# Kernel tuning notes

Measured on AMD Instinct MI355X. Metric: run time of the kernel, lower is better.

The kernel has to match this reference:

```python
import jax, jax.numpy as jnp
import numpy as np

B = 1024
N_CPGS = 20000
N_FREQS = N_CPGS // 2 + 1  # 10001
HIDDEN = (256, 128, 64)
LN_EPS = 1e-5


def setup_inputs() -> dict:
    key = jax.random.key(0)
    keys = jax.random.split(key, 16)
    inp = {"x": jax.random.normal(keys[0], (B, N_CPGS), dtype=jnp.float32)}
    in_dim = N_FREQS
    for i, h in enumerate(HIDDEN):
        inp[f"W{i}"] = jax.random.normal(keys[1 + i], (h, in_dim), dtype=jnp.float32) * 0.01
        inp[f"alpha{i}"] = jnp.full((h, in_dim), 0.01, dtype=jnp.float32)
        inp[f"b{i}"] = jnp.zeros((h,), dtype=jnp.float32)
        inp[f"eta{i}"] = jnp.asarray(0.1, dtype=jnp.float32)
        inp[f"g{i}"] = jnp.ones((h,), dtype=jnp.float32)   # LayerNorm gamma
        inp[f"be{i}"] = jnp.zeros((h,), dtype=jnp.float32)  # LayerNorm beta
        in_dim = h
    inp["head_w"] = jax.random.normal(keys[10], (1, in_dim), dtype=jnp.float32) * (1.0 / np.sqrt(in_dim))
    inp["head_b"] = jnp.zeros((1,), dtype=jnp.float32)
    return inp


def _hebbian_layer(x, W, alpha, b, eta):
    # y_slow = x W^T + b;  plastic[b,i] = eta * tanh(y_slow)[b,i] * sum_j sigmoid(alpha)[i,j] * x_norm[b,j] * x[b,j]
    y_slow = jnp.einsum('bd,hd->bh', x, W) + b
    x_norm = x / (jnp.linalg.norm(x, axis=-1, keepdims=True) + 1e-8)
    c = x_norm * x  # (B, in) -- collapses the (B,out,in) outer-product trace algebraically
    plastic = eta * jnp.tanh(y_slow) * jnp.einsum('bd,hd->bh', c, jax.nn.sigmoid(alpha))
    return y_slow + plastic


def _layer_norm(h, g, be):
    mu = jnp.mean(h, axis=-1, keepdims=True)
    var = jnp.mean((h - mu) ** 2, axis=-1, keepdims=True)
    return (h - mu) * jax.lax.rsqrt(var + LN_EPS) * g + be


def reference(x, W0, alpha0, b0, eta0, g0, be0,
              W1, alpha1, b1, eta1, g1, be1,
              W2, alpha2, b2, eta2, g2, be2,
              head_w, head_b):
    # FFT spectral front-end
    xc = x - jnp.mean(x, axis=1, keepdims=True)
    h = jnp.log1p(jnp.abs(jnp.fft.rfft(xc, axis=1)))  # (B, N_FREQS)
    params = [(W0, alpha0, b0, eta0, g0, be0),
              (W1, alpha1, b1, eta1, g1, be1),
              (W2, alpha2, b2, eta2, g2, be2)]
    for (W, a, b, eta, g, be) in params:
        h = jax.nn.gelu(_layer_norm(_hebbian_layer(h, W, a, b, eta), g, be), approximate=False)
        # dropout is identity in eval mode
    return (jnp.einsum('bd,od->bo', h, head_w) + head_b)[:, 0]  # (B,)
```

## Files before the change

kernel.cpp:

```cpp
#include <hip/hip_runtime.h>
#include <hip/hip_bf16.h>
#include <math.h>

typedef short bf16x8 __attribute__((ext_vector_type(8)));
typedef float f32x4 __attribute__((ext_vector_type(4)));

static __device__ __forceinline__ unsigned short f2bf(float f) {
    unsigned int u = __float_as_uint(f);
    unsigned int r = (u + 0x7fffu + ((u >> 16) & 1u)) >> 16;
    return (unsigned short)r;
}

static __device__ __forceinline__ bf16x8 sq_bf16x8(bf16x8 a) {
    bf16x8 r;
    #pragma unroll
    for (int i = 0; i < 8; ++i) {
        unsigned int u = ((unsigned int)(unsigned short)a[i]) << 16;
        float f = __uint_as_float(u);
        f *= f;
        r[i] = (short)f2bf(f);
    }
    return r;
}

static __device__ __forceinline__ float gelu_f(float x) {
    return 0.5f * x * (1.f + erff(x * 0.70710678118654752f));
}

static __device__ __forceinline__ void gload_lds16(const void* g, void* l) {
    __builtin_amdgcn_global_load_lds(
        (const __attribute__((address_space(1))) unsigned int*)g,
        (__attribute__((address_space(3))) unsigned int*)l, 16, 0, 0);
}

static __device__ __forceinline__ int ldsmap(int i) { return i + (i >> 6); }

static __device__ __forceinline__ int rev4(int k) {
    int d0 = k % 10; k /= 10;
    int d1 = k % 10; k /= 10;
    int d2 = k % 10; int d3 = k / 10;
    return d0 * 1000 + d1 * 100 + d2 * 10 + d3;
}

__global__ __launch_bounds__(256)
void init_tables_kernel(unsigned int* __restrict__ idxTab, float2* __restrict__ twAll)
{
    int i = blockIdx.x * 256 + threadIdx.x;
    if (i < 10001) {
        int k1 = (i == 10000) ? 0 : i;
        int k2 = (k1 == 0) ? 0 : 10000 - k1;
        unsigned a = (unsigned)ldsmap(rev4(k1));
        unsigned b = (unsigned)ldsmap(rev4(k2));
        idxTab[i] = a | (b << 16);
    }
    if (i < 9990) {
        int m;
        if (i < 9000)       { int t = i / 1000 + 1; int j = i - (t - 1) * 1000; m = j * t; }
        else if (i < 9900)  { int e = i - 9000; int t = e / 100 + 1; int j = e - (t - 1) * 100; m = 10 * j * t; }
        else                { int e = i - 9900; int t = e / 10 + 1;  int j = e - (t - 1) * 10;  m = 100 * j * t; }
        double ang = (double)m * -6.2831853071795864769e-4;
        twAll[i] = make_float2((float)cos(ang), (float)sin(ang));
    }
}

static __device__ __forceinline__ void dft5(
    float a0r, float a0i, float a1r, float a1i, float a2r, float a2i,
    float a3r, float a3i, float a4r, float a4i,
    float* Xr, float* Xi)
{
    const float c1 = 0.30901699437494742f, c2 = -0.80901699437494745f;
    const float s1 = 0.95105651629515357f, s2 = 0.58778525229247312f;
    float t1r = a1r + a4r, t1i = a1i + a4i;
    float d1r = a1r - a4r, d1i = a1i - a4i;
    float t2r = a2r + a3r, t2i = a2i + a3i;
    float d2r = a2r - a3r, d2i = a2i - a3i;
    Xr[0] = a0r + t1r + t2r; Xi[0] = a0i + t1i + t2i;
    float m1r = a0r + c1 * t1r + c2 * t2r, m1i = a0i + c1 * t1i + c2 * t2i;
    float m2r = a0r + c2 * t1r + c1 * t2r, m2i = a0i + c2 * t1i + c1 * t2i;
    float n1r = s1 * d1r + s2 * d2r, n1i = s1 * d1i + s2 * d2i;
    float n2r = s2 * d1r - s1 * d2r, n2i = s2 * d1i - s1 * d2i;
    Xr[1] = m1r + n1i; Xi[1] = m1i - n1r;
    Xr[4] = m1r - n1i; Xi[4] = m1i + n1r;
    Xr[2] = m2r + n2i; Xi[2] = m2i - n2r;
    Xr[3] = m2r - n2i; Xi[3] = m2i + n2r;
}

template<int S>
static __device__ __forceinline__ void radix10_core(
    float* __restrict__ reb, float* __restrict__ imb,
    const float* ar, const float* ai, int base, int j,
    const float2* __restrict__ tw)
{
    constexpr int L  = (S == 0) ? 1000 : (S == 1) ? 100 : (S == 2) ? 10 : 1;
    constexpr bool TW = (S != 3);

    const float WR[5] = {1.f, 0.80901699437494745f, 0.30901699437494742f,
                         -0.30901699437494742f, -0.80901699437494745f};
    const float WI[5] = {0.f, -0.58778525229247312f, -0.95105651629515357f,
                         -0.95105651629515357f, -0.58778525229247312f};

    float Er[5], Ei[5], Or[5], Oi[5];
    dft5(ar[0], ai[0], ar[2], ai[2], ar[4], ai[4], ar[6], ai[6], ar[8], ai[8], Er, Ei);
    dft5(ar[1], ai[1], ar[3], ai[3], ar[5], ai[5], ar[7], ai[7], ar[9], ai[9], Or, Oi);
    #pragma unroll
    for (int k = 1; k < 5; ++k) {
        float tr = Or[k] * WR[k] - Oi[k] * WI[k];
        Oi[k] = Or[k] * WI[k] + Oi[k] * WR[k];
        Or[k] = tr;
    }

    if (TW) {
        float twr[10], twi[10];
        #pragma unroll
        for (int t = 1; t < 10; ++t) {
            float2 w_ = tw[(t - 1) * L + j];
            twr[t] = w_.x; twi[t] = w_.y;
        }
        #pragma unroll
        for (int k = 0; k < 5; ++k) {
            float xr0 = Er[k] + Or[k], xi0 = Ei[k] + Oi[k];
            float xr1 = Er[k] - Or[k], xi1 = Ei[k] - Oi[k];
            int i0 = ldsmap(base + k * L);
            int i1 = ldsmap(base + (k + 5) * L);
            if (k == 0) {
                reb[i0] = xr0;
                imb[i0] = xi0;
            } else {
                reb[i0] = xr0 * twr[k] - xi0 * twi[k];
                imb[i0] = xr0 * twi[k] + xi0 * twr[k];
            }
            reb[i1] = xr1 * twr[k + 5] - xi1 * twi[k + 5];
            imb[i1] = xr1 * twi[k + 5] + xi1 * twr[k + 5];
        }
    } else {
        #pragma unroll
        for (int k = 0; k < 5; ++k) {
            int i0 = ldsmap(base + k * L);
            int i1 = ldsmap(base + (k + 5) * L);
            reb[i0] = Er[k] + Or[k]; imb[i0] = Ei[k] + Oi[k];
            reb[i1] = Er[k] - Or[k]; imb[i1] = Ei[k] - Oi[k];
        }
    }
}

template<int S>
static __device__ __forceinline__ void radix10_stage(
    float* __restrict__ reb, float* __restrict__ imb, int tid,
    const float2* __restrict__ tw)
{
    constexpr int L = (S == 1) ? 100 : (S == 2) ? 10 : 1;
    for (int w = tid; w < 1000; w += 512) {
        int g, j;
        if (S == 3) { g = w; j = 0; }
        else        { g = w / L; j = w - g * L; }
        const int base = g * (10 * L) + j;
        float ar[10], ai[10];
        #pragma unroll
        for (int u = 0; u < 10; ++u) {
            int idx = ldsmap(base + u * L);
            ar[u] = reb[idx];
            ai[u] = imb[idx];
        }
        radix10_core<S>(reb, imb, ar, ai, base, j, tw);
    }
}

__global__ __launch_bounds__(512, 4)
void fft_prep_kernel(const float* __restrict__ x,
                     unsigned short* __restrict__ hb,
                     float* __restrict__ hnorm,
                     const float* __restrict__ W0, const float* __restrict__ A0,
                     unsigned short* __restrict__ Wb, unsigned short* __restrict__ Sb,
                     const float* __restrict__ W1, const float* __restrict__ A1,
                     const float* __restrict__ W2, const float* __restrict__ A2,
                     float* __restrict__ W1T, float* __restrict__ S1T,
                     float* __restrict__ W2T, float* __restrict__ S2T,
                     const unsigned int* __restrict__ idxTab,
                     const float2* __restrict__ twAll)
{
    if (blockIdx.x >= 1024) {
        int idx = (blockIdx.x - 1024) * 512 + threadIdx.x;
        if (idx < 1280128) {
            const bool isW = idx < 640064;
            const int f4 = isW ? idx : idx - 640064;
            const float* src = isW ? W0 : A0;
            unsigned short* dst = isW ? Wb : Sb;
            float4 v = ((const float4*)src)[f4];
            float e[4] = {v.x, v.y, v.z, v.w};
            int flat = f4 * 4;
            int row = flat / 10001;
            int col = flat - row * 10001;
            #pragma unroll
            for (int i = 0; i < 4; ++i) {
                if (col == 10001) { row++; col = 0; }
                float val = isW ? e[i] : 1.f / (1.f + expf(-e[i]));
                dst[(size_t)row * 10240 + col] = f2bf(val);
                col++;
            }
        } else if (idx < 1341312) {
            int i = idx - 1280128;
            int row = i / 239;
            int col = 10001 + (i - row * 239);
            Wb[(size_t)row * 10240 + col] = 0;
            Sb[(size_t)row * 10240 + col] = 0;
        } else if (idx < 1423232) {
            int o = idx - 1341312;
            if (o < 32768) {
                int d = o >> 7, h = o & 127;
                W1T[o] = W1[h * 256 + d];
            } else if (o < 65536) {
                int p = o - 32768;
                int d = p >> 7, h = p & 127;
                S1T[p] = 1.f / (1.f + expf(-A1[h * 256 + d]));
            } else if (o < 73728) {
                int p = o - 65536;
                int d = p >> 6, h = p & 63;
                W2T[p] = W2[h * 128 + d];
            } else {
                int p = o - 73728;
                int d = p >> 6, h = p & 63;
                S2T[p] = 1.f / (1.f + expf(-A2[h * 128 + d]));
            }
        }
        return;
    }

    __shared__ float reb[10156];
    __shared__ float imb[10156];
    __shared__ float redbuf[8];

    const int b = blockIdx.x;
    const int tid = threadIdx.x;
    const int lane = tid & 63;
    const int wv = tid >> 6;

    const float2* T0 = twAll;
    const float2* T1 = twAll + 9000;
    const float2* T2 = twAll + 9900;

    const float2* z2 = (const float2*)(x + (size_t)b * 20000);
    for (int w = tid; w < 1000; w += 512) {
        float ar[10], ai[10];
        #pragma unroll
        for (int u = 0; u < 10; ++u) {
            float2 v = z2[w + u * 1000];
            ar[u] = v.x; ai[u] = v.y;
        }
        radix10_core<0>(reb, imb, ar, ai, w, w, T0);
    }
    __syncthreads();
    radix10_stage<1>(reb, imb, tid, T1);
    __syncthreads();
    radix10_stage<2>(reb, imb, tid, T2);
    __syncthreads();
    radix10_stage<3>(reb, imb, tid, (const float2*)nullptr);
    __syncthreads();

    float ct, st;
    __sincosf((float)tid * -3.14159265358979324e-4f, &st, &ct);
    const float RC = 0.987091579f;
    const float RS = -0.160156842f;
    float sumsq = 0.f;
    unsigned short* hrow = hb + (size_t)b * 10240;
    #pragma unroll
    for (int i = 0; i < 20; ++i) {
        int k = tid + i * 512;
        float hval = 0.f;
        if (k > 0 && k <= 10000) {
            unsigned pp = idxTab[k];
            int i1 = (int)(pp & 0xffffu);
            int i2 = (int)(pp >> 16);
            float zr = reb[i1], zi = imb[i1];
            float wr = reb[i2], wi = imb[i2];
            float er = 0.5f * (zr + wr);
            float ei = 0.5f * (zi - wi);
            float odr = 0.5f * (zi + wi);
            float odi = -0.5f * (zr - wr);
            float xre = er + ct * odr - st * odi;
            float xim = ei + ct * odi + st * odr;
            hval = __logf(1.f + sqrtf(xre * xre + xim * xim));
        }
        hrow[k] = f2bf(hval);
        sumsq += hval * hval;
        float nct = ct * RC - st * RS;
        st = ct * RS + st * RC;
        ct = nct;
    }
    #pragma unroll
    for (int o = 32; o; o >>= 1) sumsq += __shfl_xor(sumsq, o);
    __syncthreads();
    if (lane == 0) redbuf[wv] = sumsq;
    __syncthreads();
    if (tid == 0) {
        float tsq = 0.f;
        #pragma unroll
        for (int i = 0; i < 8; ++i) tsq += redbuf[i];
        hnorm[b] = 1.f / (sqrtf(tsq) + 1e-8f);
    }
}

__global__ __launch_bounds__(256, 3)
void gemm0_kernel(const unsigned short* __restrict__ hb,
                  const unsigned short* __restrict__ Wb, const unsigned short* __restrict__ Sb,
                  float* __restrict__ Py, float* __restrict__ Pp)
{
    __shared__ unsigned short Ah[64 * 64];
    __shared__ unsigned short Bw[64 * 64];
    __shared__ unsigned short Bs[64 * 64];

    const int t = threadIdx.x;
    const int lin = blockIdx.x;
    const int z = lin & 7;
    const int tile = lin >> 3;
    const int b0 = (tile & 15) * 64;
    const int n0 = (tile >> 4) * 64;

    const int lane = t & 63;
    const int wv = t >> 6;
    const int ml = lane & 15;
    const int q4 = lane >> 4;
    const int s0 = q4 ^ (ml & 7);

    const int sub8 = lane >> 3;
    const int sl = lane & 7;
    const int gsw = sl ^ sub8;

    f32x4 accY[4], accP[4];
    #pragma unroll
    for (int nt = 0; nt < 4; ++nt) {
        accY[nt] = (f32x4){0.f, 0.f, 0.f, 0.f};
        accP[nt] = (f32x4){0.f, 0.f, 0.f, 0.f};
    }

    const int kbase = z * 1280;

    for (int step = 0; step < 20; ++step) {
        const int k0 = kbase + step * 64;
        __syncthreads();
        #pragma unroll
        for (int j = 0; j < 2; ++j) {
            const int c = wv * 2 + j;
            const size_t goA = (size_t)(b0 + c * 8 + sub8) * 10240 + k0 + gsw * 8;
            gload_lds16(&hb[goA], &Ah[c * 512]);
            const size_t goB = (size_t)(n0 + c * 8 + sub8) * 10240 + k0 + gsw * 8;
            gload_lds16(&Wb[goB], &Bw[c * 512]);
            gload_lds16(&Sb[goB], &Bs[c * 512]);
        }
        __syncthreads();

        #pragma unroll
        for (int kk = 0; kk < 2; ++kk) {
            const int slot = (s0 ^ (kk << 2)) << 3;
            bf16x8 ah, ac, bw[4], bs[4];
            const int mrow = wv * 16 + ml;
            ah = *(const bf16x8*)&Ah[mrow * 64 + slot];
            ac = sq_bf16x8(ah);
            #pragma unroll
            for (int nt = 0; nt < 4; ++nt) {
                int nrow = nt * 16 + ml;
                bw[nt] = *(const bf16x8*)&Bw[nrow * 64 + slot];
                bs[nt] = *(const bf16x8*)&Bs[nrow * 64 + slot];
            }
            #pragma unroll
            for (int nt = 0; nt < 4; ++nt) {
                accY[nt] = __builtin_amdgcn_mfma_f32_16x16x32_bf16(ah, bw[nt], accY[nt], 0, 0, 0);
                accP[nt] = __builtin_amdgcn_mfma_f32_16x16x32_bf16(ac, bs[nt], accP[nt], 0, 0, 0);
            }
        }
    }

    const int rq = q4 * 4;
    #pragma unroll
    for (int nt = 0; nt < 4; ++nt)
        #pragma unroll
        for (int r = 0; r < 4; ++r) {
            int m = b0 + wv * 16 + rq + r;
            int n = n0 + nt * 16 + ml;
            size_t o = ((size_t)z * 1024 + m) * 256 + n;
            Py[o] = accY[nt][r];
            Pp[o] = accP[nt][r];
        }
}

__global__ __launch_bounds__(256)
void combine_tail_kernel(const float* __restrict__ Py, const float* __restrict__ Pp,
                 const float* __restrict__ hnorm,
                 const float* __restrict__ b0v, const float* __restrict__ eta0p,
                 const float* __restrict__ g0, const float* __restrict__ be0,
                 const float* __restrict__ W1T, const float* __restrict__ S1T,
                 const float* __restrict__ b1, const float* __restrict__ eta1p,
                 const float* __restrict__ g1, const float* __restrict__ be1,
                 const float* __restrict__ W2T, const float* __restrict__ S2T,
                 const float* __restrict__ b2, const float* __restrict__ eta2p,
                 const float* __restrict__ g2, const float* __restrict__ be2,
                 const float* __restrict__ hw, const float* __restrict__ hbod,
                 float* __restrict__ out)
{
    __shared__ float sh[2][256];
    __shared__ float sc[2][256];
    __shared__ float sv[2][128];
    __shared__ float sh2[2][128];
    __shared__ float sc2[2][128];
    __shared__ float sv2[2][64];
    __shared__ float p2a[2][2][64];
    __shared__ float p2b[2][2][64];
    __shared__ float redA[4][2];
    __shared__ float redB[4][2];

    const int t = threadIdx.x;
    const int b0 = blockIdx.x * 2;
    const int lane = t & 63;
    const int wv = t >> 6;

    const float e0 = eta0p[0];
    const float bias0 = b0v[t];
    float ys[2] = {0.f, 0.f}, ps[2] = {0.f, 0.f};
    #pragma unroll 4
    for (int s = 0; s < 8; ++s)
        #pragma unroll
        for (int r = 0; r < 2; ++r) {
            size_t o = ((size_t)s * 1024 + b0 + r) * 256 + t;
            ys[r] += Py[o];
            ps[r] += Pp[o];
        }
    float v[2];
    #pragma unroll
    for (int r = 0; r < 2; ++r) {
        float p = ps[r] * hnorm[b0 + r];
        float y = ys[r] + bias0;
        v[r] = y + e0 * tanhf(y) * p;
    }

    float s1[2], s2[2];
    #pragma unroll
    for (int r = 0; r < 2; ++r) { s1[r] = v[r]; s2[r] = v[r] * v[r]; }
    #pragma unroll
    for (int o = 32; o; o >>= 1)
        #pragma unroll
        for (int r = 0; r < 2; ++r) { s1[r] += __shfl_xor(s1[r], o); s2[r] += __shfl_xor(s2[r], o); }
    if (lane == 0)
        #pragma unroll
        for (int r = 0; r < 2; ++r) { redA[wv][r] = s1[r]; redB[wv][r] = s2[r]; }
    __syncthreads();

    const float gg = g0[t], bb = be0[t];
    float gl[2], s3[2];
    #pragma unroll
    for (int r = 0; r < 2; ++r) {
        float sum = redA[0][r] + redA[1][r] + redA[2][r] + redA[3][r];
        float sumsq = redB[0][r] + redB[1][r] + redB[2][r] + redB[3][r];
        float mu = sum * (1.f / 256.f);
        float var = sumsq * (1.f / 256.f) - mu * mu;
        float u = (v[r] - mu) * rsqrtf(var + 1e-5f) * gg + bb;
        gl[r] = gelu_f(u);
        s3[r] = gl[r] * gl[r];
    }
    #pragma unroll
    for (int o = 32; o; o >>= 1)
        #pragma unroll
        for (int r = 0; r < 2; ++r) s3[r] += __shfl_xor(s3[r], o);
    __syncthreads();
    if (lane == 0)
        #pragma unroll
        for (int r = 0; r < 2; ++r) redA[wv][r] = s3[r];
    __syncthreads();
    #pragma unroll
    for (int r = 0; r < 2; ++r) {
        float gsq = redA[0][r] + redA[1][r] + redA[2][r] + redA[3][r];
        float inv = 1.f / (sqrtf(gsq) + 1e-8f);
        sh[r][t] = gl[r];
        sc[r][t] = gl[r] * gl[r] * inv;
    }
    __syncthreads();

    const int hcol = t & 127;
    const int r1 = t >> 7;
    float ya = 0.f, pa = 0.f;
    #pragma unroll 8
    for (int d = 0; d < 256; ++d) {
        ya += sh[r1][d] * W1T[d * 128 + hcol];
        pa += sc[r1][d] * S1T[d * 128 + hcol];
    }
    {
        const float e1 = eta1p[0];
        float y = ya + b1[hcol];
        sv[r1][hcol] = y + e1 * tanhf(y) * pa;
    }
    __syncthreads();

    if (wv < 2) {
        int r = wv;
        float v0 = sv[r][lane];
        float v1 = sv[r][lane + 64];
        float s = v0 + v1, sq = v0 * v0 + v1 * v1;
        #pragma unroll
        for (int o = 32; o; o >>= 1) { s += __shfl_xor(s, o); sq += __shfl_xor(sq, o); }
        float mu = s * (1.f / 128.f);
        float var = sq * (1.f / 128.f) - mu * mu;
        float rs = rsqrtf(var + 1e-5f);
        float u0 = (v0 - mu) * rs * g1[lane] + be1[lane];
        float u1 = (v1 - mu) * rs * g1[lane + 64] + be1[lane + 64];
        float ge0 = gelu_f(u0);
        float ge1 = gelu_f(u1);
        float gsq = ge0 * ge0 + ge1 * ge1;
        #pragma unroll
        for (int o = 32; o; o >>= 1) gsq += __shfl_xor(gsq, o);
        float inv = 1.f / (sqrtf(gsq) + 1e-8f);
        sh2[r][lane] = ge0; sh2[r][lane + 64] = ge1;
        sc2[r][lane] = ge0 * ge0 * inv; sc2[r][lane + 64] = ge1 * ge1 * inv;
    }
    __syncthreads();

    {
        const int h2c = t & 63;
        const int r = (t >> 6) & 1;
        const int dh = t >> 7;
        float yb = 0.f, pb = 0.f;
        #pragma unroll 8
        for (int dd = 0; dd < 64; ++dd) {
            int d = dh * 64 + dd;
            yb += sh2[r][d] * W2T[d * 64 + h2c];
            pb += sc2[r][d] * S2T[d * 64 + h2c];
        }
        p2a[dh][r][h2c] = yb;
        p2b[dh][r][h2c] = pb;
    }
    __syncthreads();
    if (t < 128) {
        const int h2c = t & 63;
        const int r = t >> 6;
        const float e2 = eta2p[0];
        float yb = p2a[0][r][h2c] + p2a[1][r][h2c];
        float pb = p2b[0][r][h2c] + p2b[1][r][h2c];
        float y = yb + b2[h2c];
        sv2[r][h2c] = y + e2 * tanhf(y) * pb;
    }
    __syncthreads();

    if (wv < 2) {
        int r = wv;
        float v0 = sv2[r][lane];
        float s = v0, sq = v0 * v0;
        #pragma unroll
        for (int o = 32; o; o >>= 1) { s += __shfl_xor(s, o); sq += __shfl_xor(sq, o); }
        float mu = s * (1.f / 64.f);
        float var = sq * (1.f / 64.f) - mu * mu;
        float rs = rsqrtf(var + 1e-5f);
        float u = (v0 - mu) * rs * g2[lane] + be2[lane];
        float g = gelu_f(u);
        float hc = g * hw[lane];
        #pragma unroll
        for (int o = 32; o; o >>= 1) hc += __shfl_xor(hc, o);
        if (lane == 0) out[b0 + r] = hc + hbod[0];
    }
}

extern "C" void kernel_launch(void* const* d_in, const int* in_sizes, int n_in,
                              void* d_out, int out_size, void* d_ws, size_t ws_size,
                              hipStream_t stream)
{
    const float* x    = (const float*)d_in[0];
    const float* W0   = (const float*)d_in[1];
    const float* A0   = (const float*)d_in[2];
    const float* b0   = (const float*)d_in[3];
    const float* eta0 = (const float*)d_in[4];
    const float* g0   = (const float*)d_in[5];
    const float* be0  = (const float*)d_in[6];
    const float* W1   = (const float*)d_in[7];
    const float* A1   = (const float*)d_in[8];
    const float* b1   = (const float*)d_in[9];
    const float* eta1 = (const float*)d_in[10];
    const float* g1   = (const float*)d_in[11];
    const float* be1  = (const float*)d_in[12];
    const float* W2   = (const float*)d_in[13];
    const float* A2   = (const float*)d_in[14];
    const float* b2   = (const float*)d_in[15];
    const float* eta2 = (const float*)d_in[16];
    const float* g2   = (const float*)d_in[17];
    const float* be2  = (const float*)d_in[18];
    const float* hw   = (const float*)d_in[19];
    const float* hbod = (const float*)d_in[20];
    float* out = (float*)d_out;

    char* w = (char*)d_ws;
    unsigned short* hb  = (unsigned short*)(w + 0);
    unsigned short* Wb0 = (unsigned short*)(w + 20971520);
    unsigned short* Sb0 = (unsigned short*)(w + 26214400);
    float* Py   = (float*)(w + 31457280);
    float* Pp   = (float*)(w + 39845888);
    float* W1T  = (float*)(w + 48234496);
    float* S1T  = (float*)(w + 48365568);
    float* W2T  = (float*)(w + 48496640);
    float* S2T  = (float*)(w + 48529408);
    float* hnm  = (float*)(w + 48562176);
    unsigned int* idxT = (unsigned int*)(w + 48566272);
    float2* twT = (float2*)(w + 48607232);

    hipLaunchKernelGGL(init_tables_kernel, dim3(40), dim3(256), 0, stream, idxT, twT);
    hipLaunchKernelGGL(fft_prep_kernel, dim3(3804), dim3(512), 0, stream,
                       x, hb, hnm, W0, A0, Wb0, Sb0, W1, A1, W2, A2, W1T, S1T, W2T, S2T,
                       idxT, twT);
    hipLaunchKernelGGL(gemm0_kernel, dim3(512), dim3(256), 0, stream, hb, Wb0, Sb0, Py, Pp);
    hipLaunchKernelGGL(combine_tail_kernel, dim3(512), dim3(256), 0, stream, Py, Pp, hnm,
                       b0, eta0, g0, be0, W1T, S1T, b1, eta1, g1, be1,
                       W2T, S2T, b2, eta2, g2, be2, hw, hbod, out);
}
```

Before: 255.3 us.

## Fuse GEMM and tail via cooperative grid sync; compute FFT twiddles inline

Removes the twiddle/index table init kernel and computes twiddles on the fly with sincos plus a recurrence, and computes the bit-reverse indices inline. The GEMM and the combine/tail kernels are merged into one cooperative kernel with a grid-wide sync in between, so two launches disappear. The cooperative launch needs all 512 blocks resident at once and lowers launch_bounds occupancy to 2. Twiddle accuracy may drop slightly because of fast sincos and the recurrence.

```diff
diff --git a/kernel.cpp b/kernel.cpp
--- a/kernel.cpp
+++ b/kernel.cpp
@@ -1,6 +1,9 @@
 #include <hip/hip_runtime.h>
 #include <hip/hip_bf16.h>
+#include <hip/hip_cooperative_groups.h>
 #include <math.h>
+
+namespace cg = cooperative_groups;
 
 typedef short bf16x8 __attribute__((ext_vector_type(8)));
 typedef float f32x4 __attribute__((ext_vector_type(4)));
@@ -40,27 +43,6 @@
     int d1 = k % 10; k /= 10;
     int d2 = k % 10; int d3 = k / 10;
     return d0 * 1000 + d1 * 100 + d2 * 10 + d3;
-}
-
-__global__ __launch_bounds__(256)
-void init_tables_kernel(unsigned int* __restrict__ idxTab, float2* __restrict__ twAll)
-{
-    int i = blockIdx.x * 256 + threadIdx.x;
-    if (i < 10001) {
-        int k1 = (i == 10000) ? 0 : i;
-        int k2 = (k1 == 0) ? 0 : 10000 - k1;
-        unsigned a = (unsigned)ldsmap(rev4(k1));
-        unsigned b = (unsigned)ldsmap(rev4(k2));
-        idxTab[i] = a | (b << 16);
-    }
-    if (i < 9990) {
-        int m;
-        if (i < 9000)       { int t = i / 1000 + 1; int j = i - (t - 1) * 1000; m = j * t; }
-        else if (i < 9900)  { int e = i - 9000; int t = e / 100 + 1; int j = e - (t - 1) * 100; m = 10 * j * t; }
-        else                { int e = i - 9900; int t = e / 10 + 1;  int j = e - (t - 1) * 10;  m = 100 * j * t; }
-        double ang = (double)m * -6.2831853071795864769e-4;
-        twAll[i] = make_float2((float)cos(ang), (float)sin(ang));
-    }
 }
 
 static __device__ __forceinline__ void dft5(
@@ -88,10 +70,10 @@
 template<int S>
 static __device__ __forceinline__ void radix10_core(
     float* __restrict__ reb, float* __restrict__ imb,
-    const float* ar, const float* ai, int base, int j,
-    const float2* __restrict__ tw)
+    const float* ar, const float* ai, int base, int j)
 {
     constexpr int L  = (S == 0) ? 1000 : (S == 1) ? 100 : (S == 2) ? 10 : 1;
+    constexpr int SC = (S == 0) ? 1 : (S == 1) ? 10 : (S == 2) ? 100 : 1000;
     constexpr bool TW = (S != 3);
 
     const float WR[5] = {1.f, 0.80901699437494745f, 0.30901699437494742f,
@@ -110,11 +92,15 @@
     }
 
     if (TW) {
+        const float ang = (float)(j * SC) * -6.28318530717958648e-4f;
+        float w1c, w1s;
+        __sincosf(ang, &w1s, &w1c);
         float twr[10], twi[10];
+        twr[0] = 1.f; twi[0] = 0.f;
         #pragma unroll
         for (int t = 1; t < 10; ++t) {
-            float2 w_ = tw[(t - 1) * L + j];
-            twr[t] = w_.x; twi[t] = w_.y;
+            twr[t] = twr[t - 1] * w1c - twi[t - 1] * w1s;
+            twi[t] = twr[t - 1] * w1s + twi[t - 1] * w1c;
         }
         #pragma unroll
         for (int k = 0; k < 5; ++k) {
@@ -145,8 +131,7 @@
 
 template<int S>
 static __device__ __forceinline__ void radix10_stage(
-    float* __restrict__ reb, float* __restrict__ imb, int tid,
-    const float2* __restrict__ tw)
+    float* __restrict__ reb, float* __restrict__ imb, int tid)
 {
     constexpr int L = (S == 1) ? 100 : (S == 2) ? 10 : 1;
     for (int w = tid; w < 1000; w += 512) {
@@ -161,7 +146,7 @@
             ar[u] = reb[idx];
             ai[u] = imb[idx];
         }
-        radix10_core<S>(reb, imb, ar, ai, base, j, tw);
+        radix10_core<S>(reb, imb, ar, ai, base, j);
     }
 }
 
@@ -174,9 +159,7 @@
                      const float* __restrict__ W1, const float* __restrict__ A1,
                      const float* __restrict__ W2, const float* __restrict__ A2,
                      float* __restrict__ W1T, float* __restrict__ S1T,
-                     float* __restrict__ W2T, float* __restrict__ S2T,
-                     const unsigned int* __restrict__ idxTab,
-                     const float2* __restrict__ twAll)
+                     float* __restrict__ W2T, float* __restrict__ S2T)
 {
     if (blockIdx.x >= 1024) {
         int idx = (blockIdx.x - 1024) * 512 + threadIdx.x;
@@ -234,10 +217,6 @@
     const int lane = tid & 63;
     const int wv = tid >> 6;
 
-    const float2* T0 = twAll;
-    const float2* T1 = twAll + 9000;
-    const float2* T2 = twAll + 9900;
-
     const float2* z2 = (const float2*)(x + (size_t)b * 20000);
     for (int w = tid; w < 1000; w += 512) {
         float ar[10], ai[10];
@@ -246,20 +225,16 @@
             float2 v = z2[w + u * 1000];
             ar[u] = v.x; ai[u] = v.y;
         }
-        radix10_core<0>(reb, imb, ar, ai, w, w, T0);
+        radix10_core<0>(reb, imb, ar, ai, w, w);
     }
     __syncthreads();
-    radix10_stage<1>(reb, imb, tid, T1);
+    radix10_stage<1>(reb, imb, tid);
     __syncthreads();
-    radix10_stage<2>(reb, imb, tid, T2);
+    radix10_stage<2>(reb, imb, tid);
     __syncthreads();
-    radix10_stage<3>(reb, imb, tid, (const float2*)nullptr);
+    radix10_stage<3>(reb, imb, tid);
     __syncthreads();
 
-    float ct, st;
-    __sincosf((float)tid * -3.14159265358979324e-4f, &st, &ct);
-    const float RC = 0.987091579f;
-    const float RS = -0.160156842f;
     float sumsq = 0.f;
     unsigned short* hrow = hb + (size_t)b * 10240;
     #pragma unroll
@@ -267,24 +242,24 @@
         int k = tid + i * 512;
         float hval = 0.f;
         if (k > 0 && k <= 10000) {
-            unsigned pp = idxTab[k];
-            int i1 = (int)(pp & 0xffffu);
-            int i2 = (int)(pp >> 16);
+            int k1 = (k == 10000) ? 0 : k;
+            int k2 = (k1 == 0) ? 0 : 10000 - k1;
+            int i1 = ldsmap(rev4(k1));
+            int i2 = ldsmap(rev4(k2));
             float zr = reb[i1], zi = imb[i1];
             float wr = reb[i2], wi = imb[i2];
             float er = 0.5f * (zr + wr);
             float ei = 0.5f * (zi - wi);
             float odr = 0.5f * (zi + wi);
             float odi = -0.5f * (zr - wr);
+            float ct, st;
+            __sincosf((float)k * -3.14159265358979324e-4f, &st, &ct);
             float xre = er + ct * odr - st * odi;
             float xim = ei + ct * odi + st * odr;
             hval = __logf(1.f + sqrtf(xre * xre + xim * xim));
         }
         hrow[k] = f2bf(hval);
         sumsq += hval * hval;
-        float nct = ct * RC - st * RS;
-        st = ct * RS + st * RC;
-        ct = nct;
     }
     #pragma unroll
     for (int o = 32; o; o >>= 1) sumsq += __shfl_xor(sumsq, o);
@@ -299,103 +274,26 @@
     }
 }
 
-__global__ __launch_bounds__(256, 3)
-void gemm0_kernel(const unsigned short* __restrict__ hb,
-                  const unsigned short* __restrict__ Wb, const unsigned short* __restrict__ Sb,
-                  float* __restrict__ Py, float* __restrict__ Pp)
+__global__ __launch_bounds__(256, 2)
+void gemm_tail_kernel(const unsigned short* __restrict__ hb,
+                      const unsigned short* __restrict__ Wb, const unsigned short* __restrict__ Sb,
+                      float* __restrict__ Py, float* __restrict__ Pp,
+                      const float* __restrict__ hnorm,
+                      const float* __restrict__ b0v, const float* __restrict__ eta0p,
+                      const float* __restrict__ g0, const float* __restrict__ be0,
+                      const float* __restrict__ W1T, const float* __restrict__ S1T,
+                      const float* __restrict__ b1, const float* __restrict__ eta1p,
+                      const float* __restrict__ g1, const float* __restrict__ be1,
+                      const float* __restrict__ W2T, const float* __restrict__ S2T,
+                      const float* __restrict__ b2, const float* __restrict__ eta2p,
+                      const float* __restrict__ g2, const float* __restrict__ be2,
+                      const float* __restrict__ hw, const float* __restrict__ hbod,
+                      float* __restrict__ out)
 {
     __shared__ unsigned short Ah[64 * 64];
     __shared__ unsigned short Bw[64 * 64];
     __shared__ unsigned short Bs[64 * 64];
 
-    const int t = threadIdx.x;
-    const int lin = blockIdx.x;
-    const int z = lin & 7;
-    const int tile = lin >> 3;
-    const int b0 = (tile & 15) * 64;
-    const int n0 = (tile >> 4) * 64;
-
-    const int lane = t & 63;
-    const int wv = t >> 6;
-    const int ml = lane & 15;
-    const int q4 = lane >> 4;
-    const int s0 = q4 ^ (ml & 7);
-
-    const int sub8 = lane >> 3;
-    const int sl = lane & 7;
-    const int gsw = sl ^ sub8;
-
-    f32x4 accY[4], accP[4];
-    #pragma unroll
-    for (int nt = 0; nt < 4; ++nt) {
-        accY[nt] = (f32x4){0.f, 0.f, 0.f, 0.f};
-        accP[nt] = (f32x4){0.f, 0.f, 0.f, 0.f};
-    }
-
-    const int kbase = z * 1280;
-
-    for (int step = 0; step < 20; ++step) {
-        const int k0 = kbase + step * 64;
-        __syncthreads();
-        #pragma unroll
-        for (int j = 0; j < 2; ++j) {
-            const int c = wv * 2 + j;
-            const size_t goA = (size_t)(b0 + c * 8 + sub8) * 10240 + k0 + gsw * 8;
-            gload_lds16(&hb[goA], &Ah[c * 512]);
-            const size_t goB = (size_t)(n0 + c * 8 + sub8) * 10240 + k0 + gsw * 8;
-            gload_lds16(&Wb[goB], &Bw[c * 512]);
-            gload_lds16(&Sb[goB], &Bs[c * 512]);
-        }
-        __syncthreads();
-
-        #pragma unroll
-        for (int kk = 0; kk < 2; ++kk) {
-            const int slot = (s0 ^ (kk << 2)) << 3;
-            bf16x8 ah, ac, bw[4], bs[4];
-            const int mrow = wv * 16 + ml;
-            ah = *(const bf16x8*)&Ah[mrow * 64 + slot];
-            ac = sq_bf16x8(ah);
-            #pragma unroll
-            for (int nt = 0; nt < 4; ++nt) {
-                int nrow = nt * 16 + ml;
-                bw[nt] = *(const bf16x8*)&Bw[nrow * 64 + slot];
-                bs[nt] = *(const bf16x8*)&Bs[nrow * 64 + slot];
-            }
-            #pragma unroll
-            for (int nt = 0; nt < 4; ++nt) {
-                accY[nt] = __builtin_amdgcn_mfma_f32_16x16x32_bf16(ah, bw[nt], accY[nt], 0, 0, 0);
-                accP[nt] = __builtin_amdgcn_mfma_f32_16x16x32_bf16(ac, bs[nt], accP[nt], 0, 0, 0);
-            }
-        }
-    }
-
-    const int rq = q4 * 4;
-    #pragma unroll
-    for (int nt = 0; nt < 4; ++nt)
-        #pragma unroll
-        for (int r = 0; r < 4; ++r) {
-            int m = b0 + wv * 16 + rq + r;
-            int n = n0 + nt * 16 + ml;
-            size_t o = ((size_t)z * 1024 + m) * 256 + n;
-            Py[o] = accY[nt][r];
-            Pp[o] = accP[nt][r];
-        }
-}
-
-__global__ __launch_bounds__(256)
-void combine_tail_kernel(const float* __restrict__ Py, const float* __restrict__ Pp,
-                 const float* __restrict__ hnorm,
-                 const float* __restrict__ b0v, const float* __restrict__ eta0p,
-                 const float* __restrict__ g0, const float* __restrict__ be0,
-                 const float* __restrict__ W1T, const float* __restrict__ S1T,
-                 const float* __restrict__ b1, const float* __restrict__ eta1p,
-                 const float* __restrict__ g1, const float* __restrict__ be1,
-                 const float* __restrict__ W2T, const float* __restrict__ S2T,
-                 const float* __restrict__ b2, const float* __restrict__ eta2p,
-                 const float* __restrict__ g2, const float* __restrict__ be2,
-                 const float* __restrict__ hw, const float* __restrict__ hbod,
-                 float* __restrict__ out)
-{
     __shared__ float sh[2][256];
     __shared__ float sc[2][256];
     __shared__ float sv[2][128];
@@ -408,150 +306,227 @@
     __shared__ float redB[4][2];
 
     const int t = threadIdx.x;
-    const int b0 = blockIdx.x * 2;
     const int lane = t & 63;
     const int wv = t >> 6;
 
-    const float e0 = eta0p[0];
-    const float bias0 = b0v[t];
-    float ys[2] = {0.f, 0.f}, ps[2] = {0.f, 0.f};
-    #pragma unroll 4
-    for (int s = 0; s < 8; ++s)
+    {
+        const int lin = blockIdx.x;
+        const int z = lin & 7;
+        const int tile = lin >> 3;
+        const int b0 = (tile & 15) * 64;
+        const int n0 = (tile >> 4) * 64;
+
+        const int ml = lane & 15;
+        const int q4 = lane >> 4;
+        const int s0 = q4 ^ (ml & 7);
+        const int sub8 = lane >> 3;
+        const int sl = lane & 7;
+        const int gsw = sl ^ sub8;
+
+        f32x4 accY[4], accP[4];
+        #pragma unroll
+        for (int nt = 0; nt < 4; ++nt) {
+            accY[nt] = (f32x4){0.f, 0.f, 0.f, 0.f};
+            accP[nt] = (f32x4){0.f, 0.f, 0.f, 0.f};
+        }
+
+        const int kbase = z * 1280;
+
+        for (int step = 0; step < 20; ++step) {
+            const int k0 = kbase + step * 64;
+            __syncthreads();
+            #pragma unroll
+            for (int j = 0; j < 2; ++j) {
+                const int c = wv * 2 + j;
+                const size_t goA = (size_t)(b0 + c * 8 + sub8) * 10240 + k0 + gsw * 8;
+                gload_lds16(&hb[goA], &Ah[c * 512]);
+                const size_t goB = (size_t)(n0 + c * 8 + sub8) * 10240 + k0 + gsw * 8;
+                gload_lds16(&Wb[goB], &Bw[c * 512]);
+                gload_lds16(&Sb[goB], &Bs[c * 512]);
+            }
+            __syncthreads();
+
+            #pragma unroll
+            for (int kk = 0; kk < 2; ++kk) {
+                const int slot = (s0 ^ (kk << 2)) << 3;
+                bf16x8 ah, ac, bw[4], bs[4];
+                const int mrow = wv * 16 + ml;
+                ah = *(const bf16x8*)&Ah[mrow * 64 + slot];
+                ac = sq_bf16x8(ah);
+                #pragma unroll
+                for (int nt = 0; nt < 4; ++nt) {
+                    int nrow = nt * 16 + ml;
+                    bw[nt] = *(const bf16x8*)&Bw[nrow * 64 + slot];
+                    bs[nt] = *(const bf16x8*)&Bs[nrow * 64 + slot];
+                }
+                #pragma unroll
+                for (int nt = 0; nt < 4; ++nt) {
+                    accY[nt] = __builtin_amdgcn_mfma_f32_16x16x32_bf16(ah, bw[nt], accY[nt], 0, 0, 0);
+                    accP[nt] = __builtin_amdgcn_mfma_f32_16x16x32_bf16(ac, bs[nt], accP[nt], 0, 0, 0);
+                }
+            }
+        }
+
+        const int rq = q4 * 4;
+        #pragma unroll
+        for (int nt = 0; nt < 4; ++nt)
+            #pragma unroll
+            for (int r = 0; r < 4; ++r) {
+                int m = b0 + wv * 16 + rq + r;
+                int n = n0 + nt * 16 + ml;
+                size_t o = ((size_t)z * 1024 + m) * 256 + n;
+                Py[o] = accY[nt][r];
+                Pp[o] = accP[nt][r];
+            }
+    }
+
+    __threadfence();
+    cg::this_grid().sync();
+
+    {
+        const int b0 = blockIdx.x * 2;
+
+        const float e0 = eta0p[0];
+        const float bias0 = b0v[t];
+        float ys[2] = {0.f, 0.f}, ps[2] = {0.f, 0.f};
+        #pragma unroll 4
+        for (int s = 0; s < 8; ++s)
+            #pragma unroll
+            for (int r = 0; r < 2; ++r) {
+                size_t o = ((size_t)s * 1024 + b0 + r) * 256 + t;
+                ys[r] += Py[o];
+                ps[r] += Pp[o];
+            }
+        float v[2];
         #pragma unroll
         for (int r = 0; r < 2; ++r) {
-            size_t o = ((size_t)s * 1024 + b0 + r) * 256 + t;
-            ys[r] += Py[o];
-            ps[r] += Pp[o];
-        }
-    float v[2];
-    #pragma unroll
-    for (int r = 0; r < 2; ++r) {
-        float p = ps[r] * hnorm[b0 + r];
-        float y = ys[r] + bias0;
-        v[r] = y + e0 * tanhf(y) * p;
-    }
-
-    float s1[2], s2[2];
-    #pragma unroll
-    for (int r = 0; r < 2; ++r) { s1[r] = v[r]; s2[r] = v[r] * v[r]; }
-    #pragma unroll
-    for (int o = 32; o; o >>= 1)
-        #pragma unroll
-        for (int r = 0; r < 2; ++r) { s1[r] += __shfl_xor(s1[r], o); s2[r] += __shfl_xor(s2[r], o); }
-    if (lane == 0)
-        #pragma unroll
-        for (int r = 0; r < 2; ++r) { redA[wv][r] = s1[r]; redB[wv][r] = s2[r]; }
-    __syncthreads();
-
-    const float gg = g0[t], bb = be0[t];
-    float gl[2], s3[2];
-    #pragma unroll
-    for (int r = 0; r < 2; ++r) {
-        float sum = redA[0][r] + redA[1][r] + redA[2][r] + redA[3][r];
-        float sumsq = redB[0][r] + redB[1][r] + redB[2][r] + redB[3][r];
-        float mu = sum * (1.f / 256.f);
-        float var = sumsq * (1.f / 256.f) - mu * mu;
-        float u = (v[r] - mu) * rsqrtf(var + 1e-5f) * gg + bb;
-        gl[r] = gelu_f(u);
-        s3[r] = gl[r] * gl[r];
-    }
-    #pragma unroll
-    for (int o = 32; o; o >>= 1)
-        #pragma unroll
-        for (int r = 0; r < 2; ++r) s3[r] += __shfl_xor(s3[r], o);
-    __syncthreads();
-    if (lane == 0)
-        #pragma unroll
-        for (int r = 0; r < 2; ++r) redA[wv][r] = s3[r];
-    __syncthreads();
-    #pragma unroll
-    for (int r = 0; r < 2; ++r) {
-        float gsq = redA[0][r] + redA[1][r] + redA[2][r] + redA[3][r];
-        float inv = 1.f / (sqrtf(gsq) + 1e-8f);
-        sh[r][t] = gl[r];
-        sc[r][t] = gl[r] * gl[r] * inv;
-    }
-    __syncthreads();
-
-    const int hcol = t & 127;
-    const int r1 = t >> 7;
-    float ya = 0.f, pa = 0.f;
-    #pragma unroll 8
-    for (int d = 0; d < 256; ++d) {
-        ya += sh[r1][d] * W1T[d * 128 + hcol];
-        pa += sc[r1][d] * S1T[d * 128 + hcol];
-    }
-    {
-        const float e1 = eta1p[0];
-        float y = ya + b1[hcol];
-        sv[r1][hcol] = y + e1 * tanhf(y) * pa;
-    }
-    __syncthreads();
-
-    if (wv < 2) {
-        int r = wv;
-        float v0 = sv[r][lane];
-        float v1 = sv[r][lane + 64];
-        float s = v0 + v1, sq = v0 * v0 + v1 * v1;
-        #pragma unroll
-        for (int o = 32; o; o >>= 1) { s += __shfl_xor(s, o); sq += __shfl_xor(sq, o); }
-        float mu = s * (1.f / 128.f);
-        float var = sq * (1.f / 128.f) - mu * mu;
-        float rs = rsqrtf(var + 1e-5f);
-        float u0 = (v0 - mu) * rs * g1[lane] + be1[lane];
-        float u1 = (v1 - mu) * rs * g1[lane + 64] + be1[lane + 64];
-        float ge0 = gelu_f(u0);
-        float ge1 = gelu_f(u1);
-        float gsq = ge0 * ge0 + ge1 * ge1;
-        #pragma unroll
-        for (int o = 32; o; o >>= 1) gsq += __shfl_xor(gsq, o);
-        float inv = 1.f / (sqrtf(gsq) + 1e-8f);
-        sh2[r][lane] = ge0; sh2[r][lane + 64] = ge1;
-        sc2[r][lane] = ge0 * ge0 * inv; sc2[r][lane + 64] = ge1 * ge1 * inv;
-    }
-    __syncthreads();
-
-    {
-        const int h2c = t & 63;
-        const int r = (t >> 6) & 1;
-        const int dh = t >> 7;
-        float yb = 0.f, pb = 0.f;
+            float p = ps[r] * hnorm[b0 + r];
+            float y = ys[r] + bias0;
+            v[r] = y + e0 * tanhf(y) * p;
+        }
+
+        float s1[2], s2[2];
+        #pragma unroll
+        for (int r = 0; r < 2; ++r) { s1[r] = v[r]; s2[r] = v[r] * v[r]; }
+        #pragma unroll
+        for (int o = 32; o; o >>= 1)
+            #pragma unroll
+            for (int r = 0; r < 2; ++r) { s1[r] += __shfl_xor(s1[r], o); s2[r] += __shfl_xor(s2[r], o); }
+        if (lane == 0)
+            #pragma unroll
+            for (int r = 0; r < 2; ++r) { redA[wv][r] = s1[r]; redB[wv][r] = s2[r]; }
+        __syncthreads();
+
+        const float gg = g0[t], bb = be0[t];
+        float gl[2], s3[2];
+        #pragma unroll
+        for (int r = 0; r < 2; ++r) {
+            float sum = redA[0][r] + redA[1][r] + redA[2][r] + redA[3][r];
+            float sumsq = redB[0][r] + redB[1][r] + redB[2][r] + redB[3][r];
+            float mu = sum * (1.f / 256.f);
+            float var = sumsq * (1.f / 256.f) - mu * mu;
+            float u = (v[r] - mu) * rsqrtf(var + 1e-5f) * gg + bb;
+            gl[r] = gelu_f(u);
+            s3[r] = gl[r] * gl[r];
+        }
+        #pragma unroll
+        for (int o = 32; o; o >>= 1)
+            #pragma unroll
+            for (int r = 0; r < 2; ++r) s3[r] += __shfl_xor(s3[r], o);
+        __syncthreads();
+        if (lane == 0)
+            #pragma unroll
+            for (int r = 0; r < 2; ++r) redA[wv][r] = s3[r];
+        __syncthreads();
+        #pragma unroll
+        for (int r = 0; r < 2; ++r) {
+            float gsq = redA[0][r] + redA[1][r] + redA[2][r] + redA[3][r];
+            float inv = 1.f / (sqrtf(gsq) + 1e-8f);
+            sh[r][t] = gl[r];
+            sc[r][t] = gl[r] * gl[r] * inv;
+        }
+        __syncthreads();
+
+        const int hcol = t & 127;
+        const int r1 = t >> 7;
+        float ya = 0.f, pa = 0.f;
         #pragma unroll 8
-        for (int dd = 0; dd < 64; ++dd) {
-            int d = dh * 64 + dd;
-            yb += sh2[r][d] * W2T[d * 64 + h2c];
-            pb += sc2[r][d] * S2T[d * 64 + h2c];
-        }
-        p2a[dh][r][h2c] = yb;
-        p2b[dh][r][h2c] = pb;
-    }
-    __syncthreads();
-    if (t < 128) {
-        const int h2c = t & 63;
-        const int r = t >> 6;
-        const float e2 = eta2p[0];
-        float yb = p2a[0][r][h2c] + p2a[1][r][h2c];
-        float pb = p2b[0][r][h2c] + p2b[1][r][h2c];
-        float y = yb + b2[h2c];
-        sv2[r][h2c] = y + e2 * tanhf(y) * pb;
-    }
-    __syncthreads();
-
-    if (wv < 2) {
-        int r = wv;
-        float v0 = sv2[r][lane];
-        float s = v0, sq = v0 * v0;
-        #pragma unroll
-        for (int o = 32; o; o >>= 1) { s += __shfl_xor(s, o); sq += __shfl_xor(sq, o); }
-        float mu = s * (1.f / 64.f);
-        float var = sq * (1.f / 64.f) - mu * mu;
-        float rs = rsqrtf(var + 1e-5f);
-        float u = (v0 - mu) * rs * g2[lane] + be2[lane];
-        float g = gelu_f(u);
-        float hc = g * hw[lane];
-        #pragma unroll
-        for (int o = 32; o; o >>= 1) hc += __shfl_xor(hc, o);
-        if (lane == 0) out[b0 + r] = hc + hbod[0];
+        for (int d = 0; d < 256; ++d) {
+            ya += sh[r1][d] * W1T[d * 128 + hcol];
+            pa += sc[r1][d] * S1T[d * 128 + hcol];
+        }
+        {
+            const float e1 = eta1p[0];
+            float y = ya + b1[hcol];
+            sv[r1][hcol] = y + e1 * tanhf(y) * pa;
+        }
+        __syncthreads();
+
+        if (wv < 2) {
+            int r = wv;
+            float v0 = sv[r][lane];
+            float v1 = sv[r][lane + 64];
+            float s = v0 + v1, sq = v0 * v0 + v1 * v1;
+            #pragma unroll
+            for (int o = 32; o; o >>= 1) { s += __shfl_xor(s, o); sq += __shfl_xor(sq, o); }
+            float mu = s * (1.f / 128.f);
+            float var = sq * (1.f / 128.f) - mu * mu;
+            float rs = rsqrtf(var + 1e-5f);
+            float u0 = (v0 - mu) * rs * g1[lane] + be1[lane];
+            float u1 = (v1 - mu) * rs * g1[lane + 64] + be1[lane + 64];
+            float ge0 = gelu_f(u0);
+            float ge1 = gelu_f(u1);
+            float gsq = ge0 * ge0 + ge1 * ge1;
+            #pragma unroll
+            for (int o = 32; o; o >>= 1) gsq += __shfl_xor(gsq, o);
+            float inv = 1.f / (sqrtf(gsq) + 1e-8f);
+            sh2[r][lane] = ge0; sh2[r][lane + 64] = ge1;
+            sc2[r][lane] = ge0 * ge0 * inv; sc2[r][lane + 64] = ge1 * ge1 * inv;
+        }
+        __syncthreads();
+
+        {
+            const int h2c = t & 63;
+            const int r = (t >> 6) & 1;
+            const int dh = t >> 7;
+            float yb = 0.f, pb = 0.f;
+            #pragma unroll 8
+            for (int dd = 0; dd < 64; ++dd) {
+                int d = dh * 64 + dd;
+                yb += sh2[r][d] * W2T[d * 64 + h2c];
+                pb += sc2[r][d] * S2T[d * 64 + h2c];
+            }
+            p2a[dh][r][h2c] = yb;
+            p2b[dh][r][h2c] = pb;
+        }
+        __syncthreads();
+        if (t < 128) {
+            const int h2c = t & 63;
+            const int r = t >> 6;
+            const float e2 = eta2p[0];
+            float yb = p2a[0][r][h2c] + p2a[1][r][h2c];
+            float pb = p2b[0][r][h2c] + p2b[1][r][h2c];
+            float y = yb + b2[h2c];
+            sv2[r][h2c] = y + e2 * tanhf(y) * pb;
+        }
+        __syncthreads();
+
+        if (wv < 2) {
+            int r = wv;
+            float v0 = sv2[r][lane];
+            float s = v0, sq = v0 * v0;
+            #pragma unroll
+            for (int o = 32; o; o >>= 1) { s += __shfl_xor(s, o); sq += __shfl_xor(sq, o); }
+            float mu = s * (1.f / 64.f);
+            float var = sq * (1.f / 64.f) - mu * mu;
+            float rs = rsqrtf(var + 1e-5f);
+            float u = (v0 - mu) * rs * g2[lane] + be2[lane];
+            float g = gelu_f(u);
+            float hc = g * hw[lane];
+            #pragma unroll
+            for (int o = 32; o; o >>= 1) hc += __shfl_xor(hc, o);
+            if (lane == 0) out[b0 + r] = hc + hbod[0];
+        }
     }
 }
 
@@ -593,15 +568,19 @@
     float* W2T  = (float*)(w + 48496640);
     float* S2T  = (float*)(w + 48529408);
     float* hnm  = (float*)(w + 48562176);
-    unsigned int* idxT = (unsigned int*)(w + 48566272);
-    float2* twT = (float2*)(w + 48607232);
-
-    hipLaunchKernelGGL(init_tables_kernel, dim3(40), dim3(256), 0, stream, idxT, twT);
+
     hipLaunchKernelGGL(fft_prep_kernel, dim3(3804), dim3(512), 0, stream,
-                       x, hb, hnm, W0, A0, Wb0, Sb0, W1, A1, W2, A2, W1T, S1T, W2T, S2T,
-                       idxT, twT);
-    hipLaunchKernelGGL(gemm0_kernel, dim3(512), dim3(256), 0, stream, hb, Wb0, Sb0, Py, Pp);
-    hipLaunchKernelGGL(combine_tail_kernel, dim3(512), dim3(256), 0, stream, Py, Pp, hnm,
-                       b0, eta0, g0, be0, W1T, S1T, b1, eta1, g1, be1,
-                       W2T, S2T, b2, eta2, g2, be2, hw, hbod, out);
-}
+                       x, hb, hnm, W0, A0, Wb0, Sb0, W1, A1, W2, A2, W1T, S1T, W2T, S2T);
+
+    void* kargs[] = {
+        (void*)&hb, (void*)&Wb0, (void*)&Sb0, (void*)&Py, (void*)&Pp,
+        (void*)&hnm,
+        (void*)&b0, (void*)&eta0, (void*)&g0, (void*)&be0,
+        (void*)&W1T, (void*)&S1T, (void*)&b1, (void*)&eta1,
+        (void*)&g1, (void*)&be1, (void*)&W2T, (void*)&S2T,
+        (void*)&b2, (void*)&eta2, (void*)&g2, (void*)&be2,
+        (void*)&hw, (void*)&hbod, (void*)&out
+    };
+    hipLaunchCooperativeKernel(reinterpret_cast<void*>(gemm_tail_kernel),
+                               dim3(512), dim3(256), kargs, 0, stream);
+}
```

Result: slower. 403.8 us (+58.2%).
